# Performance work log

Hardware: AMD Instinct MI355X
Metric: run time of the kernel (lower is better)

The kernel has to match this reference:

```python
import jax, jax.numpy as jnp
import numpy as np

IN_DIMS = (32, 64, 96, 128)
N_EXPERTS = len(IN_DIMS)
MAX_F = max(IN_DIMS)
D = 2 * MAX_F
N = 8192
TOP_K = 2
H_DIM = 1024
OUT_DIM = 768
LN_EPS = 1e-6


def _build_mask():
    # mask[f] = [1]*s + [0]*(MAX_F-s) + [1]*s + [0]*(MAX_F-s), shape (E, 1, D)
    m = np.zeros((N_EXPERTS, 1, D), dtype=np.float32)
    for i, s in enumerate(IN_DIMS):
        m[i, 0, :s] = 1.0
        m[i, 0, MAX_F:MAX_F + s] = 1.0
    return jnp.asarray(m)

_MASK = _build_mask()


def _multi_in_expert(x_final, expert_weights, expert_indices, W, b):
    """MoE dispatch/combine of MultiInSizeLinear (expert_indices path).
    x_final: (E, N, D); expert_weights/indices: (N, K); W: (E, O, D); b: (E, O)."""
    Wm = W * _MASK                                   # (E, O, D) masked per-size weights
    # per-expert outputs for every token (the torch loop computes these per mask group)
    Y = jnp.einsum('end,eod->eno', x_final, Wm) + b[:, None, :]   # (E, N, O)
    valid = expert_indices < N_EXPERTS               # (N, K) real-expert mask
    rsum = jnp.sum(expert_weights * valid, axis=-1, keepdims=True)
    rsum = jnp.where(rsum == 0, 1.0, rsum)
    wnorm = jnp.where(valid, expert_weights / rsum, 0.0)          # (N, K)
    safe = jnp.where(valid, expert_indices, 0)
    n_idx = jnp.arange(Y.shape[1])
    gathered = Y[safe, n_idx[:, None]]               # (N, K, O)
    return jnp.sum(wnorm[..., None] * gathered, axis=1)           # (N, O)


def setup_inputs() -> dict:
    key = jax.random.key(0)
    ks = jax.random.split(key, 12)
    s_hid = 1.0 / np.sqrt(D)
    s_out = 1.0 / np.sqrt(H_DIM)
    return {
        'x': jax.random.normal(ks[0], (N, D), jnp.float32),
        'in_feat_size': jax.random.randint(ks[1], (N,), 0, MAX_F, jnp.int64) if jax.config.jax_enable_x64 else jax.random.randint(ks[1], (N,), 0, MAX_F, jnp.int32),
        'expert_weights': jax.random.uniform(ks[2], (N, TOP_K), jnp.float32),
        'expert_indices': jax.random.randint(ks[3], (N, TOP_K), 0, 6, jnp.int32),
        'x_final': jax.random.normal(ks[4], (N_EXPERTS, N, D), jnp.float32),
        'W_hid': jax.random.normal(ks[5], (N_EXPERTS, H_DIM, D), jnp.float32) * s_hid,
        'b_hid': jax.random.normal(ks[6], (N_EXPERTS, H_DIM), jnp.float32) * s_hid,
        'W_out': jax.random.normal(ks[7], (OUT_DIM, H_DIM), jnp.float32) * s_out,
        'b_out': jax.random.normal(ks[8], (OUT_DIM,), jnp.float32) * s_out,
        'W_res': jax.random.normal(ks[9], (N_EXPERTS, OUT_DIM, D), jnp.float32) * s_hid,
        'b_res': jax.random.normal(ks[10], (N_EXPERTS, OUT_DIM), jnp.float32) * s_hid,
        'ln_w': jnp.ones((OUT_DIM,), jnp.float32),
    }


def reference(x, in_feat_size, expert_weights, expert_indices, x_final,
              W_hid, b_hid, W_out, b_out, W_res, b_res, ln_w):
    xf = jnp.nan_to_num(x_final, nan=0.0)
    hid = _multi_in_expert(xf, expert_weights, expert_indices, W_hid, b_hid)
    hid = jax.nn.gelu(hid, approximate=False)
    out = hid @ W_out.T + b_out                      # output_layer (dropout p=0 -> identity)
    res = _multi_in_expert(xf, expert_weights, expert_indices, W_res, b_res)
    out = out + res
    # T5LayerNorm (RMSNorm)
    var = jnp.mean(out * out, axis=-1, keepdims=True)
    return ln_w * (out * jax.lax.rsqrt(var + LN_EPS))
```

## Files before the change

### kernel.cpp

```cpp
#include <hip/hip_runtime.h>
#include <hip/hip_bf16.h>

#define TOKENS 8192
#define D_IN   256
#define HDIM   1024
#define ODIM   768
#define KPACK  704
#define NCHUNK 88

typedef short bf16x8 __attribute__((ext_vector_type(8)));
typedef float f32x4  __attribute__((ext_vector_type(4)));

static __device__ __forceinline__ ushort f2b(float f) {
    union { __hip_bfloat16 b; ushort u; } cv;
    cv.b = __float2bfloat16(f);
    return cv.u;
}
static __device__ __forceinline__ float b2f(ushort u) {
    union { ushort u; __hip_bfloat16 b; } cv;
    cv.u = u;
    return __bfloat162float(cv.b);
}

static __device__ __forceinline__ void chunk_map(int c8, int& e, int& d0) {
    int cc;
    if (c8 < 8)       { e = 0; cc = c8; }
    else if (c8 < 24) { e = 1; cc = c8 - 8; }
    else if (c8 < 48) { e = 2; cc = c8 - 24; }
    else              { e = 3; cc = c8 - 48; }
    int half = 4 * (e + 1);
    d0 = (cc < half) ? cc * 8 : 128 + (cc - half) * 8;
}

static __device__ __forceinline__ void stage16(const ushort* g, ushort* l) {
    __builtin_amdgcn_global_load_lds(
        (const __attribute__((address_space(1))) void*)g,
        (__attribute__((address_space(3))) void*)l, 16, 0, 0);
}

static __device__ __forceinline__ float gelu_f(float v) {
    float y = 0.7978845608f * v * (1.f + 0.044715f * v * v);
    return v - v / (__expf(2.f * y) + 1.f);
}

__global__ __launch_bounds__(256) void k_pack_a(
    const float* __restrict__ ew, const int* __restrict__ ei,
    const float* __restrict__ xf, ushort* __restrict__ Ap) {
    int gid = blockIdx.x * 256 + threadIdx.x;
    int n  = gid / NCHUNK;
    int c8 = gid - n * NCHUNK;
    int   i0 = ei[2 * n], i1 = ei[2 * n + 1];
    float w0 = ew[2 * n], w1 = ew[2 * n + 1];
    bool v0 = (unsigned)i0 < 4u, v1 = (unsigned)i1 < 4u;
    float rs = (v0 ? w0 : 0.f) + (v1 ? w1 : 0.f);
    if (rs == 0.f) rs = 1.f;
    float o0 = v0 ? w0 / rs : 0.f;
    float o1 = v1 ? w1 / rs : 0.f;
    ushort o[8] __attribute__((aligned(16))) = {0, 0, 0, 0, 0, 0, 0, 0};
    if (c8 < 80) {
        int e, d0;
        chunk_map(c8, e, d0);
        float w = ((v0 && i0 == e) ? o0 : 0.f) + ((v1 && i1 == e) ? o1 : 0.f);
        if (w != 0.f) {
            const float* s = xf + ((size_t)e * TOKENS + n) * D_IN + d0;
#pragma unroll
            for (int j = 0; j < 8; ++j) {
                float v = s[j];
                if (!(v == v)) v = 0.f;
                o[j] = f2b(w * v);
            }
        }
    } else if (c8 == 80) {
#pragma unroll
        for (int j = 0; j < 4; ++j) {
            float m = ((v0 && i0 == j) ? o0 : 0.f) + ((v1 && i1 == j) ? o1 : 0.f);
            o[j] = f2b(m);
        }
    }
    *(uint4*)(Ap + (size_t)n * KPACK + c8 * 8) = *(const uint4*)o;
}

#define BW_SPLIT (1792 * NCHUNK)
__global__ __launch_bounds__(256) void k_pack_bw(
    const float* __restrict__ Whid, const float* __restrict__ bhid,
    const float* __restrict__ Wres, const float* __restrict__ bres,
    const float* __restrict__ Wout,
    ushort* __restrict__ Bp, ushort* __restrict__ Wb) {
    int gid = blockIdx.x * 256 + threadIdx.x;
    if (gid < BW_SPLIT) {
        int o_ = gid / NCHUNK;
        int c8 = gid - o_ * NCHUNK;
        ushort v[8] __attribute__((aligned(16))) = {0, 0, 0, 0, 0, 0, 0, 0};
        if (c8 < 80) {
            int e, d0;
            chunk_map(c8, e, d0);
            const float* s = (o_ < HDIM)
                ? Whid + ((size_t)e * HDIM + o_) * D_IN + d0
                : Wres + ((size_t)e * ODIM + (o_ - HDIM)) * D_IN + d0;
#pragma unroll
            for (int j = 0; j < 8; ++j) v[j] = f2b(s[j]);
        } else if (c8 == 80) {
#pragma unroll
            for (int j = 0; j < 4; ++j) {
                float b = (o_ < HDIM) ? bhid[j * HDIM + o_] : bres[j * ODIM + (o_ - HDIM)];
                v[j] = f2b(b);
            }
        }
        *(uint4*)(Bp + (size_t)o_ * KPACK + c8 * 8) = *(const uint4*)v;
    } else {
        int g2 = gid - BW_SPLIT;
        const float* s = Wout + (size_t)g2 * 8;
        ushort v[8] __attribute__((aligned(16)));
#pragma unroll
        for (int j = 0; j < 8; ++j) v[j] = f2b(s[j]);
        *(uint4*)(Wb + (size_t)g2 * 8) = *(const uint4*)v;
    }
}

__global__ __launch_bounds__(512, 2) void k_gemm1(
    const ushort* __restrict__ A, const ushort* __restrict__ B,
    ushort* __restrict__ hidB, ushort* __restrict__ resb) {
    __shared__ __align__(16) ushort As[2][256 * 64];
    __shared__ __align__(16) ushort Bs[2][256 * 64];
    const int tid = threadIdx.x;
    const int lane = tid & 63, w = tid >> 6;
    const int wr = w >> 2, wc = w & 3;
    const int r = lane & 15, g = lane >> 4;
    const int sx = r & 7;

    int bid  = blockIdx.x;
    int widx = (bid & 7) * 28 + (bid >> 3);
    int bm = widx / 7, bn = widx - bm * 7;

    const int srow = tid >> 3;
    const int gc   = (tid & 7) ^ (srow & 7);
    const int wv8  = w * 8;
    const ushort* Abase = A + (size_t)(bm * 256) * KPACK;
    const ushort* Bbase = B + (size_t)(bn * 256) * KPACK;

#define STG(gsrc, grow, kc, lds, lrow)                                      \
    stage16((gsrc) + (size_t)((grow) + srow) * KPACK + ((kc) + gc) * 8,     \
            (lds) + ((lrow) + wv8) * 64)
#define STG8(p, kc) do {                                                    \
    STG(Abase, 0, kc, &As[p][0], 0);     STG(Abase, 64, kc, &As[p][0], 64); \
    STG(Abase, 128, kc, &As[p][0], 128); STG(Abase, 192, kc, &As[p][0], 192);\
    STG(Bbase, 0, kc, &Bs[p][0], 0);     STG(Bbase, 64, kc, &Bs[p][0], 64); \
    STG(Bbase, 128, kc, &Bs[p][0], 128); STG(Bbase, 192, kc, &Bs[p][0], 192);} while (0)

    STG8(0, 0);
    STG8(1, 8);
    asm volatile("s_waitcnt vmcnt(8)" ::: "memory");
    __builtin_amdgcn_s_barrier();

    f32x4 acc[8][4] = {};

#define LD_A(buf, mi, ks) (*(const bf16x8*)&As[buf][(wr * 128 + (mi) * 16 + r) * 64 + ((((ks) * 4 + g) ^ sx) * 8)])
#define LD_B(buf, j, ks)  (*(const bf16x8*)&Bs[buf][(wc * 64  + (j) * 16 + r) * 64 + ((((ks) * 4 + g) ^ sx) * 8)])
#define READ_A(buf, qq) do {                                                  \
    af[0][0] = LD_A(buf, 2 * (qq), 0);     af[0][1] = LD_A(buf, 2 * (qq), 1); \
    af[1][0] = LD_A(buf, 2 * (qq) + 1, 0); af[1][1] = LD_A(buf, 2 * (qq) + 1, 1); } while (0)
#define READ_B(buf) do { _Pragma("unroll")                                   \
    for (int j_ = 0; j_ < 4; ++j_) { bfr[j_][0] = LD_B(buf, j_, 0); bfr[j_][1] = LD_B(buf, j_, 1); } } while (0)
#define MFMA_Q(qq) do {                                                      \
    _Pragma("unroll") for (int i_ = 0; i_ < 2; ++i_)                         \
    _Pragma("unroll") for (int k_ = 0; k_ < 2; ++k_)                         \
    _Pragma("unroll") for (int j_ = 0; j_ < 4; ++j_)                         \
        acc[2 * (qq) + i_][j_] = __builtin_amdgcn_mfma_f32_16x16x32_bf16(    \
            af[i_][k_], bfr[j_][k_], acc[2 * (qq) + i_][j_], 0, 0, 0);       \
    } while (0)

#pragma unroll
    for (int t = 0; t < 11; ++t) {
        const int buf = t & 1;
        bf16x8 af[2][2], bfr[4][2];
        __builtin_amdgcn_s_setprio(1);
        READ_B(buf);
        READ_A(buf, 0); MFMA_Q(0);
        READ_A(buf, 1); MFMA_Q(1);
        READ_A(buf, 2); MFMA_Q(2);
        READ_A(buf, 3); MFMA_Q(3);
        __builtin_amdgcn_s_setprio(0);
        if (t < 10) {
            asm volatile("s_waitcnt lgkmcnt(0)" ::: "memory");
            __builtin_amdgcn_sched_barrier(0);
            __builtin_amdgcn_s_barrier();
            if (t + 2 <= 10) {
                STG8(buf, (t + 2) * 8);
                asm volatile("s_waitcnt vmcnt(8)" ::: "memory");
            } else {
                asm volatile("s_waitcnt vmcnt(0)" ::: "memory");
            }
            __builtin_amdgcn_s_barrier();
        }
    }
#undef STG
#undef STG8
#undef LD_A
#undef LD_B
#undef READ_A
#undef READ_B
#undef MFMA_Q

#pragma unroll
    for (int fi = 0; fi < 8; ++fi) {
#pragma unroll
        for (int j = 0; j < 4; ++j) {
            int col = bn * 256 + wc * 64 + j * 16 + r;
#pragma unroll
            for (int qq = 0; qq < 4; ++qq) {
                int row = bm * 256 + wr * 128 + fi * 16 + g * 4 + qq;
                float v = acc[fi][j][qq];
                if (col < HDIM) {
                    hidB[(size_t)row * HDIM + col] = f2b(gelu_f(v));
                } else {
                    resb[(size_t)row * ODIM + (col - HDIM)] = f2b(v);
                }
            }
        }
    }
}

__global__ __launch_bounds__(256, 2) void k_gemm2(
    const ushort* __restrict__ A, const ushort* __restrict__ B,
    const float* __restrict__ bout, const ushort* __restrict__ resb,
    ushort* __restrict__ outb) {
    __shared__ __align__(16) ushort As[2][128 * 64];
    __shared__ __align__(16) ushort Bs[2][128 * 64];
    const int tid = threadIdx.x;
    const int lane = tid & 63, w = tid >> 6;
    const int wr = w >> 1, wc = w & 1;
    const int r = lane & 15, g = lane >> 4;
    const int bm = blockIdx.x, bn = blockIdx.y;

    const int srow = tid >> 3;
    const int gc   = (tid & 7) ^ (srow & 7);
    const ushort* Ag = A + (size_t)(bm * 128 + srow) * HDIM + gc * 8;
    const ushort* Bg = B + (size_t)(bn * 128 + srow) * HDIM + gc * 8;
    const int ldst = (w * 8) * 64;

#define G2_STAGE(p, kt) do {                                            \
    _Pragma("unroll")                                                   \
    for (int i_ = 0; i_ < 4; ++i_) {                                    \
        stage16(Ag + (size_t)(i_ * 32) * HDIM + (kt), &As[p][ldst + i_ * 32 * 64]); \
        stage16(Bg + (size_t)(i_ * 32) * HDIM + (kt), &Bs[p][ldst + i_ * 32 * 64]); \
    } } while (0)

    G2_STAGE(0, 0);
    G2_STAGE(1, 64);

    f32x4 acc[4][4] = {};
    const int cA = (wr * 64 + r) * 64;
    const int cB = (wc * 64 + r) * 64;
    const int sx = r & 7;
    const int cs0 = ((0 * 4 + g) ^ sx) * 8;
    const int cs1 = ((1 * 4 + g) ^ sx) * 8;

    int cur = 0;
#pragma unroll
    for (int t = 0; t < 16; ++t) {
        if (t < 15) asm volatile("s_waitcnt vmcnt(8)" ::: "memory");
        else        asm volatile("s_waitcnt vmcnt(0)" ::: "memory");
        __builtin_amdgcn_s_barrier();
        const ushort* Ab = As[cur];
        const ushort* Bb = Bs[cur];
        bf16x8 a0[4], b0[4], a1[4], b1[4];
#pragma unroll
        for (int j = 0; j < 4; ++j) {
            b0[j] = *(const bf16x8*)&Bb[cB + j * 16 * 64 + cs0];
            b1[j] = *(const bf16x8*)&Bb[cB + j * 16 * 64 + cs1];
        }
#pragma unroll
        for (int i = 0; i < 4; ++i) {
            a0[i] = *(const bf16x8*)&Ab[cA + i * 16 * 64 + cs0];
            a1[i] = *(const bf16x8*)&Ab[cA + i * 16 * 64 + cs1];
        }
        asm volatile("s_waitcnt lgkmcnt(0)" ::: "memory");
        __builtin_amdgcn_sched_barrier(0);
        __builtin_amdgcn_s_barrier();
        if (t + 2 < 16) G2_STAGE(cur, (t + 2) * 64);
        __builtin_amdgcn_s_setprio(1);
#pragma unroll
        for (int i = 0; i < 4; ++i)
#pragma unroll
            for (int j = 0; j < 4; ++j)
                acc[i][j] = __builtin_amdgcn_mfma_f32_16x16x32_bf16(
                    a0[i], b0[j], acc[i][j], 0, 0, 0);
#pragma unroll
        for (int i = 0; i < 4; ++i)
#pragma unroll
            for (int j = 0; j < 4; ++j)
                acc[i][j] = __builtin_amdgcn_mfma_f32_16x16x32_bf16(
                    a1[i], b1[j], acc[i][j], 0, 0, 0);
        __builtin_amdgcn_s_setprio(0);
        cur ^= 1;
    }
#undef G2_STAGE

#pragma unroll
    for (int fi = 0; fi < 4; ++fi) {
#pragma unroll
        for (int j = 0; j < 4; ++j) {
            int col = bn * 128 + wc * 64 + j * 16 + r;
#pragma unroll
            for (int qq = 0; qq < 4; ++qq) {
                int row = bm * 128 + wr * 64 + fi * 16 + g * 4 + qq;
                size_t idx = (size_t)row * ODIM + col;
                float v = acc[fi][j][qq] + bout[col] + b2f(resb[idx]);
                outb[idx] = f2b(v);
            }
        }
    }
}

__global__ __launch_bounds__(256) void k_rms(
    const ushort* __restrict__ outb, const float* __restrict__ lnw,
    float* __restrict__ out) {
    int row = blockIdx.x, t = threadIdx.x;
    const ushort* p = outb + (size_t)row * ODIM;
    float v0 = b2f(p[t]), v1 = b2f(p[t + 256]), v2 = b2f(p[t + 512]);
    float s = v0 * v0 + v1 * v1 + v2 * v2;
#pragma unroll
    for (int off = 32; off > 0; off >>= 1) s += __shfl_down(s, off, 64);
    __shared__ float ws4[4];
    if ((t & 63) == 0) ws4[t >> 6] = s;
    __syncthreads();
    float tot = ws4[0] + ws4[1] + ws4[2] + ws4[3];
    float sc = rsqrtf(tot * (1.f / 768.f) + 1e-6f);
    out[(size_t)row * ODIM + t]       = lnw[t]       * v0 * sc;
    out[(size_t)row * ODIM + t + 256] = lnw[t + 256] * v1 * sc;
    out[(size_t)row * ODIM + t + 512] = lnw[t + 512] * v2 * sc;
}

extern "C" void kernel_launch(void* const* d_in, const int* in_sizes, int n_in,
                              void* d_out, int out_size, void* d_ws, size_t ws_size,
                              hipStream_t stream) {
    const float* ew   = (const float*)d_in[2];
    const int*   ei   = (const int*)d_in[3];
    const float* xf   = (const float*)d_in[4];
    const float* Whid = (const float*)d_in[5];
    const float* bhid = (const float*)d_in[6];
    const float* Wout = (const float*)d_in[7];
    const float* bout = (const float*)d_in[8];
    const float* Wres = (const float*)d_in[9];
    const float* bres = (const float*)d_in[10];
    const float* lnw  = (const float*)d_in[11];

    char* ws = (char*)d_ws;
    ushort* Ap   = (ushort*)(ws);
    ushort* Bp   = (ushort*)(ws + 11534336);
    ushort* Wb   = (ushort*)(ws + 14057472);
    ushort* hidB = (ushort*)(ws + 15630336);
    ushort* resb = (ushort*)(ws + 32407552);
    ushort* outb = (ushort*)(ws + 44990464);

    k_pack_a<<<2816, 256, 0, stream>>>(ew, ei, xf, Ap);
    k_pack_bw<<<1000, 256, 0, stream>>>(Whid, bhid, Wres, bres, Wout, Bp, Wb);
    k_gemm1<<<224, 512, 0, stream>>>(Ap, Bp, hidB, resb);
    k_gemm2<<<dim3(64, 6), 256, 0, stream>>>(hidB, Wb, bout, resb, outb);
    k_rms<<<8192, 256, 0, stream>>>(outb, lnw, (float*)d_out);
}
```

Baseline: 77.16 us.

## Merge pack kernels and retile GEMM1 to 128x128 blocks with 256 threads

The two packing kernels become one launch, removing a kernel boundary. GEMM1 moves from 256x256 tiles with 512 threads (224 blocks) to 128x128 tiles with 256 threads (896 blocks). Each K step now loads all fragments up front and issues the async stage before the MFMAs to overlap them. This gives better CU occupancy and load balance, at the cost of lower per-block data reuse and more global traffic.

```diff
diff --git a/kernel.cpp b/kernel.cpp
--- a/kernel.cpp
+++ b/kernel.cpp
@@ -43,53 +43,53 @@
     return v - v / (__expf(2.f * y) + 1.f);
 }
 
-__global__ __launch_bounds__(256) void k_pack_a(
+#define A_ITEMS  (TOKENS * NCHUNK)
+#define B_ITEMS  (1792 * NCHUNK)
+#define W_ITEMS  (768 * 128)
+__global__ __launch_bounds__(256) void k_pack(
     const float* __restrict__ ew, const int* __restrict__ ei,
-    const float* __restrict__ xf, ushort* __restrict__ Ap) {
-    int gid = blockIdx.x * 256 + threadIdx.x;
-    int n  = gid / NCHUNK;
-    int c8 = gid - n * NCHUNK;
-    int   i0 = ei[2 * n], i1 = ei[2 * n + 1];
-    float w0 = ew[2 * n], w1 = ew[2 * n + 1];
-    bool v0 = (unsigned)i0 < 4u, v1 = (unsigned)i1 < 4u;
-    float rs = (v0 ? w0 : 0.f) + (v1 ? w1 : 0.f);
-    if (rs == 0.f) rs = 1.f;
-    float o0 = v0 ? w0 / rs : 0.f;
-    float o1 = v1 ? w1 / rs : 0.f;
-    ushort o[8] __attribute__((aligned(16))) = {0, 0, 0, 0, 0, 0, 0, 0};
-    if (c8 < 80) {
-        int e, d0;
-        chunk_map(c8, e, d0);
-        float w = ((v0 && i0 == e) ? o0 : 0.f) + ((v1 && i1 == e) ? o1 : 0.f);
-        if (w != 0.f) {
-            const float* s = xf + ((size_t)e * TOKENS + n) * D_IN + d0;
-#pragma unroll
-            for (int j = 0; j < 8; ++j) {
-                float v = s[j];
-                if (!(v == v)) v = 0.f;
-                o[j] = f2b(w * v);
-            }
-        }
-    } else if (c8 == 80) {
-#pragma unroll
-        for (int j = 0; j < 4; ++j) {
-            float m = ((v0 && i0 == j) ? o0 : 0.f) + ((v1 && i1 == j) ? o1 : 0.f);
-            o[j] = f2b(m);
-        }
-    }
-    *(uint4*)(Ap + (size_t)n * KPACK + c8 * 8) = *(const uint4*)o;
-}
-
-#define BW_SPLIT (1792 * NCHUNK)
-__global__ __launch_bounds__(256) void k_pack_bw(
+    const float* __restrict__ xf,
     const float* __restrict__ Whid, const float* __restrict__ bhid,
     const float* __restrict__ Wres, const float* __restrict__ bres,
     const float* __restrict__ Wout,
-    ushort* __restrict__ Bp, ushort* __restrict__ Wb) {
+    ushort* __restrict__ Ap, ushort* __restrict__ Bp, ushort* __restrict__ Wb) {
     int gid = blockIdx.x * 256 + threadIdx.x;
-    if (gid < BW_SPLIT) {
-        int o_ = gid / NCHUNK;
-        int c8 = gid - o_ * NCHUNK;
+    if (gid < A_ITEMS) {
+        int n  = gid / NCHUNK;
+        int c8 = gid - n * NCHUNK;
+        int   i0 = ei[2 * n], i1 = ei[2 * n + 1];
+        float w0 = ew[2 * n], w1 = ew[2 * n + 1];
+        bool v0 = (unsigned)i0 < 4u, v1 = (unsigned)i1 < 4u;
+        float rs = (v0 ? w0 : 0.f) + (v1 ? w1 : 0.f);
+        if (rs == 0.f) rs = 1.f;
+        float o0 = v0 ? w0 / rs : 0.f;
+        float o1 = v1 ? w1 / rs : 0.f;
+        ushort o[8] __attribute__((aligned(16))) = {0, 0, 0, 0, 0, 0, 0, 0};
+        if (c8 < 80) {
+            int e, d0;
+            chunk_map(c8, e, d0);
+            float w = ((v0 && i0 == e) ? o0 : 0.f) + ((v1 && i1 == e) ? o1 : 0.f);
+            if (w != 0.f) {
+                const float* s = xf + ((size_t)e * TOKENS + n) * D_IN + d0;
+#pragma unroll
+                for (int j = 0; j < 8; ++j) {
+                    float v = s[j];
+                    if (!(v == v)) v = 0.f;
+                    o[j] = f2b(w * v);
+                }
+            }
+        } else if (c8 == 80) {
+#pragma unroll
+            for (int j = 0; j < 4; ++j) {
+                float m = ((v0 && i0 == j) ? o0 : 0.f) + ((v1 && i1 == j) ? o1 : 0.f);
+                o[j] = f2b(m);
+            }
+        }
+        *(uint4*)(Ap + (size_t)n * KPACK + c8 * 8) = *(const uint4*)o;
+    } else if (gid < A_ITEMS + B_ITEMS) {
+        int g2 = gid - A_ITEMS;
+        int o_ = g2 / NCHUNK;
+        int c8 = g2 - o_ * NCHUNK;
         ushort v[8] __attribute__((aligned(16))) = {0, 0, 0, 0, 0, 0, 0, 0};
         if (c8 < 80) {
             int e, d0;
@@ -108,112 +108,116 @@
         }
         *(uint4*)(Bp + (size_t)o_ * KPACK + c8 * 8) = *(const uint4*)v;
     } else {
-        int g2 = gid - BW_SPLIT;
-        const float* s = Wout + (size_t)g2 * 8;
+        int g3 = gid - A_ITEMS - B_ITEMS;
+        const float* s = Wout + (size_t)g3 * 8;
         ushort v[8] __attribute__((aligned(16)));
 #pragma unroll
         for (int j = 0; j < 8; ++j) v[j] = f2b(s[j]);
-        *(uint4*)(Wb + (size_t)g2 * 8) = *(const uint4*)v;
-    }
-}
-
-__global__ __launch_bounds__(512, 2) void k_gemm1(
+        *(uint4*)(Wb + (size_t)g3 * 8) = *(const uint4*)v;
+    }
+}
+
+__global__ __launch_bounds__(256, 2) void k_gemm1(
     const ushort* __restrict__ A, const ushort* __restrict__ B,
     ushort* __restrict__ hidB, ushort* __restrict__ resb) {
-    __shared__ __align__(16) ushort As[2][256 * 64];
-    __shared__ __align__(16) ushort Bs[2][256 * 64];
+    __shared__ __align__(16) ushort As[2][128 * 64];
+    __shared__ __align__(16) ushort Bs[2][128 * 64];
     const int tid = threadIdx.x;
     const int lane = tid & 63, w = tid >> 6;
-    const int wr = w >> 2, wc = w & 3;
+    const int wr = w >> 1, wc = w & 1;
     const int r = lane & 15, g = lane >> 4;
-    const int sx = r & 7;
 
     int bid  = blockIdx.x;
-    int widx = (bid & 7) * 28 + (bid >> 3);
-    int bm = widx / 7, bn = widx - bm * 7;
+    int widx = (bid & 7) * 112 + (bid >> 3);
+    int bm = widx / 14, bn = widx - bm * 14;
 
     const int srow = tid >> 3;
     const int gc   = (tid & 7) ^ (srow & 7);
-    const int wv8  = w * 8;
-    const ushort* Abase = A + (size_t)(bm * 256) * KPACK;
-    const ushort* Bbase = B + (size_t)(bn * 256) * KPACK;
-
-#define STG(gsrc, grow, kc, lds, lrow)                                      \
-    stage16((gsrc) + (size_t)((grow) + srow) * KPACK + ((kc) + gc) * 8,     \
-            (lds) + ((lrow) + wv8) * 64)
-#define STG8(p, kc) do {                                                    \
-    STG(Abase, 0, kc, &As[p][0], 0);     STG(Abase, 64, kc, &As[p][0], 64); \
-    STG(Abase, 128, kc, &As[p][0], 128); STG(Abase, 192, kc, &As[p][0], 192);\
-    STG(Bbase, 0, kc, &Bs[p][0], 0);     STG(Bbase, 64, kc, &Bs[p][0], 64); \
-    STG(Bbase, 128, kc, &Bs[p][0], 128); STG(Bbase, 192, kc, &Bs[p][0], 192);} while (0)
-
-    STG8(0, 0);
-    STG8(1, 8);
-    asm volatile("s_waitcnt vmcnt(8)" ::: "memory");
-    __builtin_amdgcn_s_barrier();
-
-    f32x4 acc[8][4] = {};
-
-#define LD_A(buf, mi, ks) (*(const bf16x8*)&As[buf][(wr * 128 + (mi) * 16 + r) * 64 + ((((ks) * 4 + g) ^ sx) * 8)])
-#define LD_B(buf, j, ks)  (*(const bf16x8*)&Bs[buf][(wc * 64  + (j) * 16 + r) * 64 + ((((ks) * 4 + g) ^ sx) * 8)])
-#define READ_A(buf, qq) do {                                                  \
-    af[0][0] = LD_A(buf, 2 * (qq), 0);     af[0][1] = LD_A(buf, 2 * (qq), 1); \
-    af[1][0] = LD_A(buf, 2 * (qq) + 1, 0); af[1][1] = LD_A(buf, 2 * (qq) + 1, 1); } while (0)
-#define READ_B(buf) do { _Pragma("unroll")                                   \
-    for (int j_ = 0; j_ < 4; ++j_) { bfr[j_][0] = LD_B(buf, j_, 0); bfr[j_][1] = LD_B(buf, j_, 1); } } while (0)
-#define MFMA_Q(qq) do {                                                      \
-    _Pragma("unroll") for (int i_ = 0; i_ < 2; ++i_)                         \
-    _Pragma("unroll") for (int k_ = 0; k_ < 2; ++k_)                         \
-    _Pragma("unroll") for (int j_ = 0; j_ < 4; ++j_)                         \
-        acc[2 * (qq) + i_][j_] = __builtin_amdgcn_mfma_f32_16x16x32_bf16(    \
-            af[i_][k_], bfr[j_][k_], acc[2 * (qq) + i_][j_], 0, 0, 0);       \
-    } while (0)
-
+    const ushort* Ag = A + (size_t)(bm * 128 + srow) * KPACK + gc * 8;
+    const ushort* Bg = B + (size_t)(bn * 128 + srow) * KPACK + gc * 8;
+    const int ldst = (w * 8) * 64;
+
+#define G1_STAGE(p, kt) do {                                            \
+    _Pragma("unroll")                                                   \
+    for (int i_ = 0; i_ < 4; ++i_) {                                    \
+        stage16(Ag + (size_t)(i_ * 32) * KPACK + (kt), &As[p][ldst + i_ * 32 * 64]); \
+        stage16(Bg + (size_t)(i_ * 32) * KPACK + (kt), &Bs[p][ldst + i_ * 32 * 64]); \
+    } } while (0)
+
+    G1_STAGE(0, 0);
+    G1_STAGE(1, 64);
+
+    f32x4 acc[4][4] = {};
+    const int cA = (wr * 64 + r) * 64;
+    const int cB = (wc * 64 + r) * 64;
+    const int sx = r & 7;
+    const int cs0 = ((0 * 4 + g) ^ sx) * 8;
+    const int cs1 = ((1 * 4 + g) ^ sx) * 8;
+
+    int cur = 0;
 #pragma unroll
     for (int t = 0; t < 11; ++t) {
-        const int buf = t & 1;
-        bf16x8 af[2][2], bfr[4][2];
+        if (t < 10) asm volatile("s_waitcnt vmcnt(8)" ::: "memory");
+        else        asm volatile("s_waitcnt vmcnt(0)" ::: "memory");
+        __builtin_amdgcn_s_barrier();
+        const ushort* Ab = As[cur];
+        const ushort* Bb = Bs[cur];
+        bf16x8 a0[4], b0[4], a1[4], b1[4];
+#pragma unroll
+        for (int j = 0; j < 4; ++j) {
+            b0[j] = *(const bf16x8*)&Bb[cB + j * 16 * 64 + cs0];
+            b1[j] = *(const bf16x8*)&Bb[cB + j * 16 * 64 + cs1];
+        }
+#pragma unroll
+        for (int i = 0; i < 4; ++i) {
+            a0[i] = *(const bf16x8*)&Ab[cA + i * 16 * 64 + cs0];
+            a1[i] = *(const bf16x8*)&Ab[cA + i * 16 * 64 + cs1];
+        }
+        asm volatile("s_waitcnt lgkmcnt(0)" ::: "memory");
+        __builtin_amdgcn_sched_barrier(0);
+        __builtin_amdgcn_s_barrier();
+        if (t + 2 < 11) G1_STAGE(cur, (t + 2) * 64);
         __builtin_amdgcn_s_setprio(1);
-        READ_B(buf);
-        READ_A(buf, 0); MFMA_Q(0);
-        READ_A(buf, 1); MFMA_Q(1);
-        READ_A(buf, 2); MFMA_Q(2);
-        READ_A(buf, 3); MFMA_Q(3);
+#pragma unroll
+        for (int i = 0; i < 4; ++i)
+#pragma unroll
+            for (int j = 0; j < 4; ++j)
+                acc[i][j] = __builtin_amdgcn_mfma_f32_16x16x32_bf16(
+                    a0[i], b0[j], acc[i][j], 0, 0, 0);
+#pragma unroll
+        for (int i = 0; i < 4; ++i)
+#pragma unroll
+            for (int j = 0; j < 4; ++j)
+                acc[i][j] = __builtin_amdgcn_mfma_f32_16x16x32_bf16(
+                    a1[i], b1[j], acc[i][j], 0, 0, 0);
         __builtin_amdgcn_s_setprio(0);
-        if (t < 10) {
-            asm volatile("s_waitcnt lgkmcnt(0)" ::: "memory");
-            __builtin_amdgcn_sched_barrier(0);
-            __builtin_amdgcn_s_barrier();
-            if (t + 2 <= 10) {
-                STG8(buf, (t + 2) * 8);
-                asm volatile("s_waitcnt vmcnt(8)" ::: "memory");
-            } else {
-                asm volatile("s_waitcnt vmcnt(0)" ::: "memory");
-            }
-            __builtin_amdgcn_s_barrier();
-        }
-    }
-#undef STG
-#undef STG8
-#undef LD_A
-#undef LD_B
-#undef READ_A
-#undef READ_B
-#undef MFMA_Q
-
-#pragma unroll
-    for (int fi = 0; fi < 8; ++fi) {
-#pragma unroll
-        for (int j = 0; j < 4; ++j) {
-            int col = bn * 256 + wc * 64 + j * 16 + r;
-#pragma unroll
-            for (int qq = 0; qq < 4; ++qq) {
-                int row = bm * 256 + wr * 128 + fi * 16 + g * 4 + qq;
-                float v = acc[fi][j][qq];
-                if (col < HDIM) {
-                    hidB[(size_t)row * HDIM + col] = f2b(gelu_f(v));
-                } else {
-                    resb[(size_t)row * ODIM + (col - HDIM)] = f2b(v);
+        cur ^= 1;
+    }
+#undef G1_STAGE
+
+    if (bn < 8) {
+#pragma unroll
+        for (int fi = 0; fi < 4; ++fi) {
+#pragma unroll
+            for (int j = 0; j < 4; ++j) {
+                int col = bn * 128 + wc * 64 + j * 16 + r;
+#pragma unroll
+                for (int qq = 0; qq < 4; ++qq) {
+                    int row = bm * 128 + wr * 64 + fi * 16 + g * 4 + qq;
+                    hidB[(size_t)row * HDIM + col] = f2b(gelu_f(acc[fi][j][qq]));
+                }
+            }
+        }
+    } else {
+#pragma unroll
+        for (int fi = 0; fi < 4; ++fi) {
+#pragma unroll
+            for (int j = 0; j < 4; ++j) {
+                int col = (bn - 8) * 128 + wc * 64 + j * 16 + r;
+#pragma unroll
+                for (int qq = 0; qq < 4; ++qq) {
+                    int row = bm * 128 + wr * 64 + fi * 16 + g * 4 + qq;
+                    resb[(size_t)row * ODIM + col] = f2b(acc[fi][j][qq]);
                 }
             }
         }
@@ -353,9 +357,9 @@
     ushort* resb = (ushort*)(ws + 32407552);
     ushort* outb = (ushort*)(ws + 44990464);
 
-    k_pack_a<<<2816, 256, 0, stream>>>(ew, ei, xf, Ap);
-    k_pack_bw<<<1000, 256, 0, stream>>>(Whid, bhid, Wres, bres, Wout, Bp, Wb);
-    k_gemm1<<<224, 512, 0, stream>>>(Ap, Bp, hidB, resb);
+    k_pack<<<3816, 256, 0, stream>>>(ew, ei, xf, Whid, bhid, Wres, bres, Wout,
+                                     Ap, Bp, Wb);
+    k_gemm1<<<896, 256, 0, stream>>>(Ap, Bp, hidB, resb);
     k_gemm2<<<dim3(64, 6), 256, 0, stream>>>(hidB, Wb, bout, resb, outb);
     k_rms<<<8192, 256, 0, stream>>>(outb, lnw, (float*)d_out);
 }
```

After: 67.76 us. -12.2%, faster.
